# Performance work log

Hardware: AMD Instinct MI355X
Metric: run time of the kernel (lower is better)

Reference implementation:

```python
import jax, jax.numpy as jnp
import numpy as np

B, T = 32, 4096
CAT, NE, HS = 128, 512, 64


def setup_inputs() -> dict:
    key = jax.random.key(0)
    ks = jax.random.split(key, 8)
    s = lambda fan_in: 1.0 / np.sqrt(fan_in)
    return {
        "x": jax.random.normal(ks[0], (B, T, NE), dtype=jnp.float32),
        "cat_emb": jax.random.normal(ks[1], (B, CAT), dtype=jnp.float32),
        # weights stored [in, out] (torch Linear weight transposed)
        "Wq": jax.random.uniform(ks[2], (CAT, HS), minval=-s(CAT), maxval=s(CAT), dtype=jnp.float32),
        "Wk": jax.random.uniform(ks[3], (NE, HS), minval=-s(NE), maxval=s(NE), dtype=jnp.float32),
        "Wv": jax.random.uniform(ks[4], (NE, HS), minval=-s(NE), maxval=s(NE), dtype=jnp.float32),
        "Wp": jax.random.uniform(ks[5], (HS, NE), minval=-s(HS), maxval=s(HS), dtype=jnp.float32),
        "gamma": jnp.ones((NE,), dtype=jnp.float32),
        "beta": jnp.zeros((NE,), dtype=jnp.float32),
    }


def reference(x, cat_emb, Wq, Wk, Wv, Wp, gamma, beta):
    # single-query cross attention: category vector attends over sequence
    q = cat_emb @ Wq                      # [B, HS]
    k = jnp.einsum("btn,nh->bth", x, Wk)  # [B, T, HS]
    v = jnp.einsum("btn,nh->bth", x, Wv)  # [B, T, HS]
    scale = 1.0 / jnp.sqrt(jnp.asarray(HS, dtype=x.dtype))
    wei = jnp.einsum("bh,bth->bt", q, k) * scale   # [B, T] scores
    wei = jax.nn.softmax(wei, axis=-1)
    out = jnp.einsum("bt,bth->bh", wei, v)         # [B, HS] attended value
    # proj + LayerNorm computed once per batch row (values are identical
    # across T since query length is 1), then broadcast to [B, T, NE]
    y = out @ Wp                                   # [B, NE]
    mu = jnp.mean(y, axis=-1, keepdims=True)
    var = jnp.mean(jnp.square(y - mu), axis=-1, keepdims=True)
    y = (y - mu) / jnp.sqrt(var + 1e-5) * gamma + beta
    return jnp.broadcast_to(y[:, None, :], (x.shape[0], x.shape[1], y.shape[-1]))
```

## Files before the change

kernel.cpp:

```cpp
#include <hip/hip_runtime.h>
#include <hip/hip_bf16.h>
#include <math.h>

#define B_   32
#define T_   4096
#define CAT_ 128
#define NE_  512
#define HS_  64

#define CHUNKS_ 32
#define RPB_ (T_ / CHUNKS_)
#define RPW_ (RPB_ / 4)

typedef float f4 __attribute__((ext_vector_type(4)));

__global__ __launch_bounds__(256, 4) void k_main(
    const float* __restrict__ x, const float* __restrict__ cat_emb,
    const float* __restrict__ Wq, const float* __restrict__ Wk,
    float* __restrict__ pm, float* __restrict__ pl, float* __restrict__ pacc)
{
    const int blk   = blockIdx.x;
    const int b     = blk >> 5;
    const int chunk = blk & 31;
    const int tid   = threadIdx.x;
    const int wave  = tid >> 6;
    const int lane  = tid & 63;

    __shared__ float sq[HS_];
    __shared__ float skq[NE_];
    __shared__ float red[256];
    __shared__ float sacc[4 * NE_];
    __shared__ float smw[4], slw[4];

    {
        const int h = tid & 63, cq = tid >> 6;
        float qp = 0.f;
        #pragma unroll 8
        for (int c = cq * 32; c < cq * 32 + 32; ++c)
            qp += cat_emb[b * CAT_ + c] * Wq[c * HS_ + h];
        red[tid] = qp;
        __syncthreads();
        if (tid < 64) sq[tid] = red[tid] + red[tid + 64] + red[tid + 128] + red[tid + 192];
        __syncthreads();
        const f4* Wk4 = (const f4*)Wk;
        const f4* sq4 = (const f4*)sq;
        #pragma unroll
        for (int half = 0; half < 2; ++half) {
            const int n = tid + half * 256;
            float acc = 0.f;
            #pragma unroll
            for (int i = 0; i < HS_ / 4; ++i) {
                const f4 w = Wk4[n * (HS_ / 4) + i];
                const f4 s = sq4[i];
                acc += w.x * s.x + w.y * s.y + w.z * s.z + w.w * s.w;
            }
            skq[n] = acc * 0.125f;
        }
        __syncthreads();
    }

    {
        const f4* kq4 = (const f4*)skq;
        const f4 kq0 = kq4[lane];
        const f4 kq1 = kq4[lane + 64];
        const float* xb = x + (size_t)b * T_ * NE_;
        const int t0 = chunk * RPB_ + wave * RPW_;

        float m = -INFINITY, l = 0.f;
        float a00 = 0.f, a01 = 0.f, a02 = 0.f, a03 = 0.f;
        float a10 = 0.f, a11 = 0.f, a12 = 0.f, a13 = 0.f;

        for (int r = 0; r < RPW_; ++r) {
            const f4* xr = (const f4*)(xb + (size_t)(t0 + r) * NE_);
            const f4 x0 = __builtin_nontemporal_load(&xr[lane]);
            const f4 x1 = __builtin_nontemporal_load(&xr[lane + 64]);
            float p = x0.x * kq0.x + x0.y * kq0.y + x0.z * kq0.z + x0.w * kq0.w
                    + x1.x * kq1.x + x1.y * kq1.y + x1.z * kq1.z + x1.w * kq1.w;
            #pragma unroll
            for (int off = 32; off >= 1; off >>= 1) p += __shfl_xor(p, off, 64);
            const float nm = fmaxf(m, p);
            const float f  = __expf(m - nm);
            const float w  = __expf(p - nm);
            m = nm;
            l = l * f + w;
            a00 = a00 * f + w * x0.x;  a01 = a01 * f + w * x0.y;
            a02 = a02 * f + w * x0.z;  a03 = a03 * f + w * x0.w;
            a10 = a10 * f + w * x1.x;  a11 = a11 * f + w * x1.y;
            a12 = a12 * f + w * x1.z;  a13 = a13 * f + w * x1.w;
        }

        if (lane == 0) { smw[wave] = m; slw[wave] = l; }
        f4* sa = (f4*)(sacc + wave * NE_);
        f4 v0; v0.x = a00; v0.y = a01; v0.z = a02; v0.w = a03;
        f4 v1; v1.x = a10; v1.y = a11; v1.z = a12; v1.w = a13;
        sa[lane]      = v0;
        sa[lane + 64] = v1;
        __syncthreads();

        const float Mb = fmaxf(fmaxf(smw[0], smw[1]), fmaxf(smw[2], smw[3]));
        const float f0 = __expf(smw[0] - Mb), f1 = __expf(smw[1] - Mb);
        const float f2 = __expf(smw[2] - Mb), f3 = __expf(smw[3] - Mb);
        float* dst = pacc + (size_t)blk * NE_;
        dst[tid]       = f0 * sacc[tid]               + f1 * sacc[NE_ + tid]
                       + f2 * sacc[2 * NE_ + tid]     + f3 * sacc[3 * NE_ + tid];
        dst[tid + 256] = f0 * sacc[tid + 256]         + f1 * sacc[NE_ + tid + 256]
                       + f2 * sacc[2 * NE_ + tid + 256] + f3 * sacc[3 * NE_ + tid + 256];
        if (tid == 0) {
            pm[blk] = Mb;
            pl[blk] = f0 * slw[0] + f1 * slw[1] + f2 * slw[2] + f3 * slw[3];
        }
    }
}

__global__ __launch_bounds__(256) void k_combine(const float* __restrict__ pm,
                                                 const float* __restrict__ pl,
                                                 const float* __restrict__ pacc,
                                                 const float* __restrict__ Wv,
                                                 const float* __restrict__ Wp,
                                                 const float* __restrict__ gamma,
                                                 const float* __restrict__ beta,
                                                 float* __restrict__ ynorm) {
    const int b   = blockIdx.x;
    const int tid = threadIdx.x;
    __shared__ float xbar[NE_];
    __shared__ float sout[HS_];
    __shared__ float red[256];

    float M = -INFINITY;
    #pragma unroll
    for (int p = 0; p < CHUNKS_; ++p) M = fmaxf(M, pm[b * CHUNKS_ + p]);
    float L = 0.f, x0 = 0.f, x1 = 0.f;
    for (int p = 0; p < CHUNKS_; ++p) {
        const float f = __expf(pm[b * CHUNKS_ + p] - M);
        L += f * pl[b * CHUNKS_ + p];
        const float* a = pacc + (size_t)(b * CHUNKS_ + p) * NE_;
        x0 += f * a[tid];
        x1 += f * a[tid + 256];
    }
    const float rL = 1.f / L;
    xbar[tid] = x0 * rL;
    xbar[tid + 256] = x1 * rL;
    __syncthreads();

    const int h = tid & 63, seg = tid >> 6;
    float o = 0.f;
    #pragma unroll 8
    for (int i = 0; i < NE_ / 4; ++i) {
        const int nn = seg * (NE_ / 4) + i;
        o += xbar[nn] * Wv[nn * HS_ + h];
    }
    red[tid] = o;
    __syncthreads();
    if (tid < 64) sout[tid] = red[tid] + red[tid + 64] + red[tid + 128] + red[tid + 192];
    __syncthreads();

    float y0 = 0.f, y1 = 0.f;
    #pragma unroll 8
    for (int hh = 0; hh < HS_; ++hh) {
        const float oh = sout[hh];
        y0 += oh * Wp[hh * NE_ + tid];
        y1 += oh * Wp[hh * NE_ + tid + 256];
    }

    red[tid] = y0 + y1;
    __syncthreads();
    for (int s = 128; s > 0; s >>= 1) { if (tid < s) red[tid] += red[tid + s]; __syncthreads(); }
    const float mu = red[0] * (1.f / NE_);
    __syncthreads();
    const float d0 = y0 - mu, d1 = y1 - mu;
    red[tid] = d0 * d0 + d1 * d1;
    __syncthreads();
    for (int s = 128; s > 0; s >>= 1) { if (tid < s) red[tid] += red[tid + s]; __syncthreads(); }
    const float rstd = rsqrtf(red[0] * (1.f / NE_) + 1e-5f);
    ynorm[b * NE_ + tid]       = d0 * rstd * gamma[tid]       + beta[tid];
    ynorm[b * NE_ + tid + 256] = d1 * rstd * gamma[tid + 256] + beta[tid + 256];
}

__global__ __launch_bounds__(256) void k_bcast(const f4* __restrict__ yn4,
                                               f4* __restrict__ out4) {
    const int blk = blockIdx.x;
    const int b   = blk >> 6;
    const int seg = blk & 63;
    const int tid = threadIdx.x;
    const f4 v = yn4[(b << 7) + (tid & 127)];
    const size_t base = ((size_t)b * T_ + (size_t)seg * 64) * (NE_ / 4);
    f4* p = out4 + base + tid;
    #pragma unroll 8
    for (int i = 0; i < 32; ++i) {
        __builtin_nontemporal_store(v, p + (size_t)i * 256);
    }
}

extern "C" void kernel_launch(void* const* d_in, const int* in_sizes, int n_in,
                              void* d_out, int out_size, void* d_ws, size_t ws_size,
                              hipStream_t stream) {
    const float* x       = (const float*)d_in[0];
    const float* cat_emb = (const float*)d_in[1];
    const float* Wq      = (const float*)d_in[2];
    const float* Wk      = (const float*)d_in[3];
    const float* Wv      = (const float*)d_in[4];
    const float* Wp      = (const float*)d_in[5];
    const float* gamma   = (const float*)d_in[6];
    const float* beta    = (const float*)d_in[7];
    float* out = (float*)d_out;

    float* ws    = (float*)d_ws;
    float* pm    = ws;
    float* pl    = pm + B_ * CHUNKS_;
    float* pacc  = pl + B_ * CHUNKS_;
    float* ynorm = pacc + (size_t)B_ * CHUNKS_ * NE_;

    k_main<<<B_ * CHUNKS_, 256, 0, stream>>>(x, cat_emb, Wq, Wk, pm, pl, pacc);
    k_combine<<<B_, 256, 0, stream>>>(pm, pl, pacc, Wv, Wp, gamma, beta, ynorm);
    k_bcast<<<2048, 256, 0, stream>>>((const f4*)ynorm, (f4*)out);
}
```

Measured before the change: 469.9 us.

## Fuse combine and broadcast kernels, process two rows per online-softmax step

The main loop now handles two sequence rows per iteration, issuing four loads up front and doing one rescale for both, which shortens the serial dependency chain and gives more memory-level parallelism. The combine kernel and broadcast kernel are merged into one 2048-block tail kernel. Each block redundantly recomputes the per-batch merge, projection and LayerNorm before writing its slice of the output. This removes a launch and the ynorm round trip, but repeats the small tail computation 64 times per batch row.

Result: no change. 472.1 us (+0.5%).

```diff
diff --git a/kernel.cpp b/kernel.cpp
--- a/kernel.cpp
+++ b/kernel.cpp
@@ -63,30 +63,43 @@
         const f4* kq4 = (const f4*)skq;
         const f4 kq0 = kq4[lane];
         const f4 kq1 = kq4[lane + 64];
-        const float* xb = x + (size_t)b * T_ * NE_;
+        const float* xbase = x + (size_t)b * T_ * NE_;
         const int t0 = chunk * RPB_ + wave * RPW_;
 
         float m = -INFINITY, l = 0.f;
         float a00 = 0.f, a01 = 0.f, a02 = 0.f, a03 = 0.f;
         float a10 = 0.f, a11 = 0.f, a12 = 0.f, a13 = 0.f;
 
-        for (int r = 0; r < RPW_; ++r) {
-            const f4* xr = (const f4*)(xb + (size_t)(t0 + r) * NE_);
-            const f4 x0 = __builtin_nontemporal_load(&xr[lane]);
-            const f4 x1 = __builtin_nontemporal_load(&xr[lane + 64]);
-            float p = x0.x * kq0.x + x0.y * kq0.y + x0.z * kq0.z + x0.w * kq0.w
-                    + x1.x * kq1.x + x1.y * kq1.y + x1.z * kq1.z + x1.w * kq1.w;
+        for (int r = 0; r < RPW_; r += 2) {
+            const f4* xrA = (const f4*)(xbase + (size_t)(t0 + r) * NE_);
+            const f4* xrB = (const f4*)(xbase + (size_t)(t0 + r + 1) * NE_);
+            const f4 xa0 = __builtin_nontemporal_load(&xrA[lane]);
+            const f4 xa1 = __builtin_nontemporal_load(&xrA[lane + 64]);
+            const f4 xb0 = __builtin_nontemporal_load(&xrB[lane]);
+            const f4 xb1 = __builtin_nontemporal_load(&xrB[lane + 64]);
+            float pa = xa0.x * kq0.x + xa0.y * kq0.y + xa0.z * kq0.z + xa0.w * kq0.w
+                     + xa1.x * kq1.x + xa1.y * kq1.y + xa1.z * kq1.z + xa1.w * kq1.w;
+            float pb = xb0.x * kq0.x + xb0.y * kq0.y + xb0.z * kq0.z + xb0.w * kq0.w
+                     + xb1.x * kq1.x + xb1.y * kq1.y + xb1.z * kq1.z + xb1.w * kq1.w;
             #pragma unroll
-            for (int off = 32; off >= 1; off >>= 1) p += __shfl_xor(p, off, 64);
-            const float nm = fmaxf(m, p);
+            for (int off = 32; off >= 1; off >>= 1) {
+                pa += __shfl_xor(pa, off, 64);
+                pb += __shfl_xor(pb, off, 64);
+            }
+            const float nm = fmaxf(fmaxf(m, pa), pb);
             const float f  = __expf(m - nm);
-            const float w  = __expf(p - nm);
+            const float wa = __expf(pa - nm);
+            const float wb = __expf(pb - nm);
             m = nm;
-            l = l * f + w;
-            a00 = a00 * f + w * x0.x;  a01 = a01 * f + w * x0.y;
-            a02 = a02 * f + w * x0.z;  a03 = a03 * f + w * x0.w;
-            a10 = a10 * f + w * x1.x;  a11 = a11 * f + w * x1.y;
-            a12 = a12 * f + w * x1.z;  a13 = a13 * f + w * x1.w;
+            l = l * f + wa + wb;
+            a00 = a00 * f + wa * xa0.x + wb * xb0.x;
+            a01 = a01 * f + wa * xa0.y + wb * xb0.y;
+            a02 = a02 * f + wa * xa0.z + wb * xb0.z;
+            a03 = a03 * f + wa * xa0.w + wb * xb0.w;
+            a10 = a10 * f + wa * xa1.x + wb * xb1.x;
+            a11 = a11 * f + wa * xa1.y + wb * xb1.y;
+            a12 = a12 * f + wa * xa1.z + wb * xb1.z;
+            a13 = a13 * f + wa * xa1.w + wb * xb1.w;
         }
 
         if (lane == 0) { smw[wave] = m; slw[wave] = l; }
@@ -112,41 +125,53 @@
     }
 }
 
-__global__ __launch_bounds__(256) void k_combine(const float* __restrict__ pm,
-                                                 const float* __restrict__ pl,
-                                                 const float* __restrict__ pacc,
-                                                 const float* __restrict__ Wv,
-                                                 const float* __restrict__ Wp,
-                                                 const float* __restrict__ gamma,
-                                                 const float* __restrict__ beta,
-                                                 float* __restrict__ ynorm) {
-    const int b   = blockIdx.x;
+__global__ __launch_bounds__(256) void k_tail(
+    const float* __restrict__ pm, const float* __restrict__ pl,
+    const float* __restrict__ pacc,
+    const float* __restrict__ Wv, const float* __restrict__ Wp,
+    const float* __restrict__ gamma, const float* __restrict__ beta,
+    f4* __restrict__ out4)
+{
+    const int blk = blockIdx.x;
+    const int b   = blk >> 6;
+    const int seg = blk & 63;
     const int tid = threadIdx.x;
+
+    __shared__ float spm[CHUNKS_], spl[CHUNKS_], sf[CHUNKS_];
     __shared__ float xbar[NE_];
     __shared__ float sout[HS_];
     __shared__ float red[256];
-
+    __shared__ __align__(16) float yn[NE_];
+
+    if (tid < CHUNKS_) { spm[tid] = pm[b * CHUNKS_ + tid]; spl[tid] = pl[b * CHUNKS_ + tid]; }
+    __syncthreads();
     float M = -INFINITY;
     #pragma unroll
-    for (int p = 0; p < CHUNKS_; ++p) M = fmaxf(M, pm[b * CHUNKS_ + p]);
-    float L = 0.f, x0 = 0.f, x1 = 0.f;
+    for (int p = 0; p < CHUNKS_; ++p) M = fmaxf(M, spm[p]);
+    if (tid < CHUNKS_) sf[tid] = __expf(spm[tid] - M);
+    __syncthreads();
+    float L = 0.f;
+    #pragma unroll
+    for (int p = 0; p < CHUNKS_; ++p) L += sf[p] * spl[p];
+    const float rL = 1.f / L;
+
+    float x0 = 0.f, x1 = 0.f;
+    #pragma unroll 4
     for (int p = 0; p < CHUNKS_; ++p) {
-        const float f = __expf(pm[b * CHUNKS_ + p] - M);
-        L += f * pl[b * CHUNKS_ + p];
+        const float f = sf[p];
         const float* a = pacc + (size_t)(b * CHUNKS_ + p) * NE_;
         x0 += f * a[tid];
         x1 += f * a[tid + 256];
     }
-    const float rL = 1.f / L;
     xbar[tid] = x0 * rL;
     xbar[tid + 256] = x1 * rL;
     __syncthreads();
 
-    const int h = tid & 63, seg = tid >> 6;
+    const int h = tid & 63, sq4 = tid >> 6;
     float o = 0.f;
     #pragma unroll 8
     for (int i = 0; i < NE_ / 4; ++i) {
-        const int nn = seg * (NE_ / 4) + i;
+        const int nn = sq4 * (NE_ / 4) + i;
         o += xbar[nn] * Wv[nn * HS_ + h];
     }
     red[tid] = o;
@@ -172,17 +197,12 @@
     __syncthreads();
     for (int s = 128; s > 0; s >>= 1) { if (tid < s) red[tid] += red[tid + s]; __syncthreads(); }
     const float rstd = rsqrtf(red[0] * (1.f / NE_) + 1e-5f);
-    ynorm[b * NE_ + tid]       = d0 * rstd * gamma[tid]       + beta[tid];
-    ynorm[b * NE_ + tid + 256] = d1 * rstd * gamma[tid + 256] + beta[tid + 256];
-}
-
-__global__ __launch_bounds__(256) void k_bcast(const f4* __restrict__ yn4,
-                                               f4* __restrict__ out4) {
-    const int blk = blockIdx.x;
-    const int b   = blk >> 6;
-    const int seg = blk & 63;
-    const int tid = threadIdx.x;
-    const f4 v = yn4[(b << 7) + (tid & 127)];
+    yn[tid]       = d0 * rstd * gamma[tid]       + beta[tid];
+    yn[tid + 256] = d1 * rstd * gamma[tid + 256] + beta[tid + 256];
+    __syncthreads();
+
+    const f4* yn4 = (const f4*)yn;
+    const f4 v = yn4[tid & 127];
     const size_t base = ((size_t)b * T_ + (size_t)seg * 64) * (NE_ / 4);
     f4* p = out4 + base + tid;
     #pragma unroll 8
@@ -204,13 +224,11 @@
     const float* beta    = (const float*)d_in[7];
     float* out = (float*)d_out;
 
-    float* ws    = (float*)d_ws;
-    float* pm    = ws;
-    float* pl    = pm + B_ * CHUNKS_;
-    float* pacc  = pl + B_ * CHUNKS_;
-    float* ynorm = pacc + (size_t)B_ * CHUNKS_ * NE_;
+    float* ws   = (float*)d_ws;
+    float* pm   = ws;
+    float* pl   = pm + B_ * CHUNKS_;
+    float* pacc = pl + B_ * CHUNKS_;
 
     k_main<<<B_ * CHUNKS_, 256, 0, stream>>>(x, cat_emb, Wq, Wk, pm, pl, pacc);
-    k_combine<<<B_, 256, 0, stream>>>(pm, pl, pacc, Wv, Wp, gamma, beta, ynorm);
-    k_bcast<<<2048, 256, 0, stream>>>((const f4*)ynorm, (f4*)out);
+    k_tail<<<2048, 256, 0, stream>>>(pm, pl, pacc, Wv, Wp, gamma, beta, (f4*)out);
 }
```
